# Performance work log

Hardware: AMD Instinct MI355X
Metric: run time of the kernel (lower is better)

Reference implementation:

```python
import jax, jax.numpy as jnp
import numpy as np

LN_EPS = 1e-5
SCALE = 1.0 / 8.0  # 1/sqrt(dim/num_heads) = 1/sqrt(64)


def layernorm(x, g, b):
    m = jnp.mean(x, axis=-1, keepdims=True)
    v = jnp.mean(jnp.square(x - m), axis=-1, keepdims=True)
    return (x - m) * jax.lax.rsqrt(v + LN_EPS) * g + b


def attention_block(q_in, kv_in, wq, bq, wk, bk, wv, bv, g, b):
    # un-split single-matrix attention, faithful to the source (no head reshape)
    Q = q_in @ wq + bq            # [B,S,D]
    K = kv_in @ wk + bk           # [B,T,D]
    V = kv_in @ wv + bv           # [B,T,D]
    scores = jnp.einsum('bsd,btd->bst', Q, K) * SCALE  # [B,S,T]
    A = jax.nn.softmax(scores, axis=-1)
    out = jnp.einsum('bst,btd->bsd', A, V)
    return layernorm(out + q_in, g, b)


def setup_inputs() -> dict:
    key = jax.random.key(0)
    ks = jax.random.split(key, 16)
    B, S, T, D = 4, 2048, 2048, 1024
    w = lambda k: jax.random.normal(k, (D, D), dtype=jnp.float32) * 0.02
    z = jnp.zeros((D,), dtype=jnp.float32)
    o = jnp.ones((D,), dtype=jnp.float32)
    return {
        'x': jax.random.normal(ks[0], (B, S, D), dtype=jnp.float32),
        'y': jax.random.normal(ks[1], (B, T, D), dtype=jnp.float32),
        'wq_m': w(ks[2]), 'bq_m': z, 'wk_m': w(ks[3]), 'bk_m': z,
        'wv_m': w(ks[4]), 'bv_m': z, 'g_m': o, 'b_m': z,
        'wq_c': w(ks[5]), 'bq_c': z, 'wk_c': w(ks[6]), 'bk_c': z,
        'wv_c': w(ks[7]), 'bv_c': z, 'g_c': o, 'b_c': z,
        'f0_w': w(ks[8]), 'f0_b': z, 'f1_w': w(ks[9]), 'f1_b': z,
        'g_d': o, 'b_d': z,
    }


def reference(x, y,
              wq_m, bq_m, wk_m, bk_m, wv_m, bv_m, g_m, b_m,
              wq_c, bq_c, wk_c, bk_c, wv_c, bv_c, g_c, b_c,
              f0_w, f0_b, f1_w, f1_b, g_d, b_d):
    # masked (self) attention + shared decoder LN residual
    res = x
    x = layernorm(attention_block(x, x, wq_m, bq_m, wk_m, bk_m, wv_m, bv_m, g_m, b_m) + res, g_d, b_d)
    # cross attention against memory y
    res = x
    x = layernorm(attention_block(x, y, wq_c, bq_c, wk_c, bk_c, wv_c, bv_c, g_c, b_c) + res, g_d, b_d)
    # FFN: loop condition in source is always true -> GELU (exact) after every layer
    res = x
    x = jax.nn.gelu(x @ f0_w + f0_b, approximate=False)
    x = jax.nn.gelu(x @ f1_w + f1_b, approximate=False)
    return layernorm(x + res, g_d, b_d)
```

## Files before the change

### kernel.cpp

```cpp
#include <hip/hip_runtime.h>

#define DEV __device__ __forceinline__

typedef __attribute__((ext_vector_type(8))) short bf16x8;
typedef __attribute__((ext_vector_type(4))) float f32x4;

DEV float bf2f(unsigned short u) { return __uint_as_float(((unsigned int)u) << 16); }
DEV unsigned short f2bf(float f) {
    unsigned int x = __float_as_uint(f);
    return (unsigned short)((x + 0x7fffu + ((x >> 16) & 1u)) >> 16);
}
DEV float gelu_exact(float x) { return 0.5f * x * (1.0f + erff(x * 0.7071067811865475f)); }

DEV void gload16(const void* g, void* l) {
    __builtin_amdgcn_global_load_lds((const __attribute__((address_space(1))) void*)g,
                                     (__attribute__((address_space(3))) void*)l, 16, 0, 0);
}

template <int OFF>
DEV bf16x8 ds_read128(unsigned addr) {
    bf16x8 r;
    asm volatile("ds_read_b128 %0, %1 offset:%2" : "=v"(r) : "v"(addr), "i"(OFF));
    return r;
}

__global__ __launch_bounds__(256) void transpose_cast_w(const float* __restrict__ in,
                                                        unsigned short* __restrict__ out,
                                                        int R, int C) {
    __shared__ float tile[32][33];
    int c0 = blockIdx.x * 32, r0 = blockIdx.y * 32;
    int tx = threadIdx.x, ty = threadIdx.y;
#pragma unroll
    for (int i = 0; i < 32; i += 8)
        tile[ty + i][tx] = in[(size_t)(r0 + ty + i) * C + (c0 + tx)];
    __syncthreads();
#pragma unroll
    for (int i = 0; i < 32; i += 8)
        out[(size_t)(c0 + ty + i) * R + (r0 + tx)] = f2bf(tile[tx][ty + i]);
}

__global__ __launch_bounds__(256) void cast_f32_bf16(const float* __restrict__ in,
                                                     unsigned short* __restrict__ out, int n4) {
    int i = blockIdx.x * 256 + threadIdx.x;
    if (i >= n4) return;
    float4 v = ((const float4*)in)[i];
    unsigned short o[4] = {f2bf(v.x), f2bf(v.y), f2bf(v.z), f2bf(v.w)};
    *(uint2*)(out + (size_t)i * 4) = *(uint2*)o;
}


template <int H>
DEV void mfma32(const bf16x8 (&a)[4][2], const bf16x8 (&b)[4][2], f32x4 (&acc)[8][4]) {
#pragma unroll
    for (int ks = 0; ks < 2; ++ks)
#pragma unroll
        for (int mi = 0; mi < 4; ++mi)
#pragma unroll
            for (int n = 0; n < 4; ++n)
                acc[4 * H + mi][n] =
                    __builtin_amdgcn_mfma_f32_16x16x32_bf16(a[mi][ks], b[n][ks], acc[4 * H + mi][n], 0, 0, 0);
}

template <int BIAS_MODE, bool GELU_ACT, bool OUT_F32>
__global__ __launch_bounds__(512, 2) void gemm256(const unsigned short* __restrict__ A,
                                                  const unsigned short* __restrict__ BT,
                                                  const float* __restrict__ bias,
                                                  float* __restrict__ Cf,
                                                  unsigned short* __restrict__ Cb,
                                                  int N, int K, int lda, int ldb, float scale,
                                                  long sA, long sB, long sC, long sBias) {
    const int gx = gridDim.x, gy = gridDim.y;
    int f = blockIdx.x + gx * (blockIdx.y + gy * blockIdx.z);
    const int nwg = gx * gy * gridDim.z;
    f = (f & 7) * (nwg >> 3) + (f >> 3);
    const int bz = f / (gx * gy);
    const int rem = f - bz * gx * gy;
    const int by = rem / gx;
    const int bx = rem - by * gx;

    A += (long)bz * sA;
    BT += (long)bz * sB;
    if (BIAS_MODE) bias += (long)bz * sBias;

    const int tid = threadIdx.x;
    const int lane = tid & 63;
    const int wave = tid >> 6;
    const int wm = wave >> 2;
    const int wn = wave & 3;
    const int llo = lane & 15, lhi = lane >> 4;
    const int bm = bx * 256, bn = by * 256;
    const int brow = (wn & 1) * 64;

    __shared__ unsigned short lds[2][4][128 * 64];

    const int xk0 = (0 + lhi) ^ (llo & 7);
    const int xk1 = (4 + lhi) ^ (llo & 7);

    const unsigned ldsA = (unsigned)(size_t)&lds[0][wm][0] + (unsigned)llo * 128u;
    const unsigned ldsB = (unsigned)(size_t)&lds[0][2 + (wn >> 1)][0] + (unsigned)(brow + llo) * 128u;
    unsigned aA[2][2], aB[2][2];
    aA[0][0] = ldsA + xk0 * 16; aA[0][1] = ldsA + xk1 * 16;
    aA[1][0] = aA[0][0] + 65536u; aA[1][1] = aA[0][1] + 65536u;
    aB[0][0] = ldsB + xk0 * 16; aB[0][1] = ldsB + xk1 * 16;
    aB[1][0] = aB[0][0] + 65536u; aB[1][1] = aB[0][1] + 65536u;

    const int d0 = wave * 64 + lane;
    const int sr0 = d0 >> 3, sq0 = (d0 & 7) ^ (sr0 & 7);
    const int d1 = 512 + d0;
    const int sr1 = d1 >> 3, sq1 = (d1 & 7) ^ (sr1 & 7);

    const unsigned short* gA0 = A + (size_t)bm * lda;
    const unsigned short* gA1 = A + (size_t)(bm + 128) * lda;
    const unsigned short* gB0 = BT + (size_t)bn * ldb;
    const unsigned short* gB1 = BT + (size_t)(bn + 128) * ldb;

#define STAGE(grow, ld, kt, l)                                                          \
    {                                                                                   \
        gload16((grow) + (size_t)sr0 * (ld) + (kt) + sq0 * 8, (l) + wave * 512);        \
        gload16((grow) + (size_t)sr1 * (ld) + (kt) + sq1 * 8, (l) + 4096 + wave * 512); \
    }
#define SA(kt, BUF) { STAGE(gA0, lda, kt, lds[BUF][0]); STAGE(gA1, lda, kt, lds[BUF][1]); }
#define SB(kt, BUF) { STAGE(gB0, ldb, kt, lds[BUF][2]); STAGE(gB1, ldb, kt, lds[BUF][3]); }

    f32x4 acc[8][4] = {};
    bf16x8 b[4][2];

#define PH2(H, BUF, LOADB, STG, TAIL)                                        \
    {                                                                        \
        STG;                                                                 \
        bf16x8 afr[4][2];                                                    \
        afr[0][0] = ds_read128<(H)*8192 + 0>(aA[BUF][0]);                    \
        afr[0][1] = ds_read128<(H)*8192 + 0>(aA[BUF][1]);                    \
        afr[1][0] = ds_read128<(H)*8192 + 2048>(aA[BUF][0]);                 \
        afr[1][1] = ds_read128<(H)*8192 + 2048>(aA[BUF][1]);                 \
        afr[2][0] = ds_read128<(H)*8192 + 4096>(aA[BUF][0]);                 \
        afr[2][1] = ds_read128<(H)*8192 + 4096>(aA[BUF][1]);                 \
        afr[3][0] = ds_read128<(H)*8192 + 6144>(aA[BUF][0]);                 \
        afr[3][1] = ds_read128<(H)*8192 + 6144>(aA[BUF][1]);                 \
        if (LOADB) {                                                         \
            b[0][0] = ds_read128<0>(aB[BUF][0]);                             \
            b[0][1] = ds_read128<0>(aB[BUF][1]);                             \
            b[1][0] = ds_read128<2048>(aB[BUF][0]);                          \
            b[1][1] = ds_read128<2048>(aB[BUF][1]);                          \
            b[2][0] = ds_read128<4096>(aB[BUF][0]);                          \
            b[2][1] = ds_read128<4096>(aB[BUF][1]);                          \
            b[3][0] = ds_read128<6144>(aB[BUF][0]);                          \
            b[3][1] = ds_read128<6144>(aB[BUF][1]);                          \
        }                                                                    \
        __builtin_amdgcn_s_barrier();                                        \
        asm volatile("s_waitcnt lgkmcnt(0)" :::);                            \
        __builtin_amdgcn_sched_barrier(0);                                   \
        __builtin_amdgcn_s_setprio(1);                                       \
        mfma32<H>(afr, b, acc);                                              \
        __builtin_amdgcn_s_setprio(0);                                       \
        TAIL;                                                                \
        __builtin_amdgcn_s_barrier();                                        \
    }

#define VM4 asm volatile("s_waitcnt vmcnt(4)" :::)
#define VM0 asm volatile("s_waitcnt vmcnt(0)" :::)
#define NOP ((void)0)

    const int nt = K >> 6;
    const int niter = nt >> 1;

    SA(0, 0);
    SB(0, 0);
    SB(64, 1);
    VM4;
    __builtin_amdgcn_s_barrier();

    int kt = 0;
    for (int i = 0; i < niter - 1; ++i) {
        const int kt1 = kt + 64, kt2 = kt + 128, kt3 = kt + 192;
        PH2(0, 0, true,  SA(kt1, 1), NOP);
        PH2(1, 0, false, SB(kt2, 0), VM4);
        PH2(0, 1, true,  SA(kt2, 0), NOP);
        PH2(1, 1, false, SB(kt3, 1), VM4);
        kt += 128;
    }
    {
        const int kt1 = kt + 64;
        PH2(0, 0, true,  SA(kt1, 1), NOP);
        PH2(1, 0, false, NOP, VM0);
        PH2(0, 1, true,  NOP, NOP);
        PH2(1, 1, false, NOP, NOP);
    }
#undef PH2
#undef SA
#undef SB
#undef STAGE
#undef VM4
#undef VM0
#undef NOP

#pragma unroll
    for (int m = 0; m < 8; ++m) {
#pragma unroll
        for (int n = 0; n < 4; ++n) {
            const int col = bn + wn * 64 + n * 16 + llo;
            float bcol = 0.f;
            if constexpr (BIAS_MODE == 1) bcol = bias[col];
#pragma unroll
            for (int j = 0; j < 4; ++j) {
                const int row = bm + wm * 128 + m * 16 + lhi * 4 + j;
                float v = acc[m][n][j] * scale + bcol;
                if constexpr (BIAS_MODE == 2) v += bias[row];
                if constexpr (GELU_ACT) v = gelu_exact(v);
                const size_t idx = (size_t)bz * (size_t)sC + (size_t)row * N + col;
                if constexpr (OUT_F32) Cf[idx] = v;
                else Cb[idx] = f2bf(v);
            }
        }
    }
}

__global__ __launch_bounds__(256) void softmax_rows(unsigned short* __restrict__ s, int T) {
    __shared__ float red[4];
    unsigned short* p = s + (size_t)blockIdx.x * T;
    const int tid = threadIdx.x;

    uint4 raw = *(const uint4*)(p + tid * 8);
    const unsigned short* u = (const unsigned short*)&raw;
    float v[8];
#pragma unroll
    for (int j = 0; j < 8; ++j) v[j] = bf2f(u[j]);

    float mx = -3.4e38f;
#pragma unroll
    for (int j = 0; j < 8; ++j) mx = fmaxf(mx, v[j]);
#pragma unroll
    for (int o = 32; o; o >>= 1) mx = fmaxf(mx, __shfl_xor(mx, o));
    if ((tid & 63) == 0) red[tid >> 6] = mx;
    __syncthreads();
    mx = fmaxf(fmaxf(red[0], red[1]), fmaxf(red[2], red[3]));
    __syncthreads();

    float sum = 0.f;
#pragma unroll
    for (int j = 0; j < 8; ++j) {
        v[j] = expf(v[j] - mx);
        sum += v[j];
    }
#pragma unroll
    for (int o = 32; o; o >>= 1) sum += __shfl_xor(sum, o);
    if ((tid & 63) == 0) red[tid >> 6] = sum;
    __syncthreads();
    sum = red[0] + red[1] + red[2] + red[3];
    const float inv = 1.0f / sum;

    unsigned short o8[8];
#pragma unroll
    for (int j = 0; j < 8; ++j) o8[j] = f2bf(v[j] * inv);
    *(uint4*)(p + tid * 8) = *(uint4*)o8;
}

DEV float block_sum(float v, float* red, int tid) {
#pragma unroll
    for (int o = 32; o; o >>= 1) v += __shfl_xor(v, o);
    if ((tid & 63) == 0) red[tid >> 6] = v;
    __syncthreads();
    v = red[0] + red[1] + red[2] + red[3];
    __syncthreads();
    return v;
}

__global__ __launch_bounds__(256) void ln_double(const float* __restrict__ av,
                                                 const float* __restrict__ xin,
                                                 const float* __restrict__ g1, const float* __restrict__ b1,
                                                 const float* __restrict__ g2, const float* __restrict__ b2,
                                                 float* __restrict__ xout,
                                                 unsigned short* __restrict__ xbf, int D) {
    __shared__ float red[4];
    const int tid = threadIdx.x;
    const size_t base = (size_t)blockIdx.x * D + tid * 4;
    const float4 a4 = *(const float4*)(av + base);
    const float4 x4 = *(const float4*)(xin + base);
    float x[4] = {x4.x, x4.y, x4.z, x4.w};
    float t[4] = {a4.x + x[0], a4.y + x[1], a4.z + x[2], a4.w + x[3]};
    const float invD = 1.0f / D;

    float m = block_sum(t[0] + t[1] + t[2] + t[3], red, tid) * invD;
    float q = 0.f;
#pragma unroll
    for (int j = 0; j < 4; ++j) q += (t[j] - m) * (t[j] - m);
    q = block_sum(q, red, tid) * invD;
    float rs = rsqrtf(q + 1e-5f);

    float u[4];
#pragma unroll
    for (int j = 0; j < 4; ++j) {
        const int idx = tid * 4 + j;
        u[j] = (t[j] - m) * rs * g1[idx] + b1[idx] + x[j];
    }
    float m2 = block_sum(u[0] + u[1] + u[2] + u[3], red, tid) * invD;
    float q2 = 0.f;
#pragma unroll
    for (int j = 0; j < 4; ++j) q2 += (u[j] - m2) * (u[j] - m2);
    q2 = block_sum(q2, red, tid) * invD;
    float rs2 = rsqrtf(q2 + 1e-5f);

    float4 o4;
    unsigned short ob[4];
#pragma unroll
    for (int j = 0; j < 4; ++j) {
        const int idx = tid * 4 + j;
        float o = (u[j] - m2) * rs2 * g2[idx] + b2[idx];
        ((float*)&o4)[j] = o;
        ob[j] = f2bf(o);
    }
    *(float4*)(xout + base) = o4;
    *(uint2*)(xbf + base) = *(uint2*)ob;
}

__global__ __launch_bounds__(256) void ln_single(const float* __restrict__ a,
                                                 const float* __restrict__ b_,
                                                 const float* __restrict__ g, const float* __restrict__ bb,
                                                 float* __restrict__ out, int D) {
    __shared__ float red[4];
    const int tid = threadIdx.x;
    const size_t base = (size_t)blockIdx.x * D + tid * 4;
    const float4 a4 = *(const float4*)(a + base);
    const float4 x4 = *(const float4*)(b_ + base);
    float t[4] = {a4.x + x4.x, a4.y + x4.y, a4.z + x4.z, a4.w + x4.w};
    const float invD = 1.0f / D;
    float m = block_sum(t[0] + t[1] + t[2] + t[3], red, tid) * invD;
    float q = 0.f;
#pragma unroll
    for (int j = 0; j < 4; ++j) q += (t[j] - m) * (t[j] - m);
    q = block_sum(q, red, tid) * invD;
    float rs = rsqrtf(q + 1e-5f);
    float4 o4;
#pragma unroll
    for (int j = 0; j < 4; ++j) {
        const int idx = tid * 4 + j;
        ((float*)&o4)[j] = (t[j] - m) * rs * g[idx] + bb[idx];
    }
    *(float4*)(out + base) = o4;
}

extern "C" void kernel_launch(void* const* d_in, const int* in_sizes, int n_in,
                              void* d_out, int out_size, void* d_ws, size_t ws_size,
                              hipStream_t stream) {
    (void)in_sizes; (void)n_in; (void)out_size; (void)ws_size;
    constexpr int B = 4, S = 2048, T = 2048, D = 1024;
    constexpr int M = B * S;
    constexpr long MD = (long)M * D;
    constexpr long ST = (long)S * T;
    constexpr long DD = (long)D * D;

    const float* x = (const float*)d_in[0];
    const float* y = (const float*)d_in[1];
    const float* w_in[8] = {(const float*)d_in[2],  (const float*)d_in[4],  (const float*)d_in[6],
                            (const float*)d_in[10], (const float*)d_in[12], (const float*)d_in[14],
                            (const float*)d_in[18], (const float*)d_in[20]};
    const float* bq_m = (const float*)d_in[3];
    const float* bk_m = (const float*)d_in[5];
    const float* bv_m = (const float*)d_in[7];
    const float* g_m = (const float*)d_in[8];
    const float* b_m = (const float*)d_in[9];
    const float* bq_c = (const float*)d_in[11];
    const float* bk_c = (const float*)d_in[13];
    const float* bv_c = (const float*)d_in[15];
    const float* g_c = (const float*)d_in[16];
    const float* b_c = (const float*)d_in[17];
    const float* f0_b = (const float*)d_in[19];
    const float* f1_b = (const float*)d_in[21];
    const float* g_d = (const float*)d_in[22];
    const float* b_d = (const float*)d_in[23];
    float* dout = (float*)d_out;

    char* p = (char*)d_ws;
    auto carve = [&](size_t bytes) { void* r = p; p += (bytes + 255) & ~(size_t)255; return r; };
    float* xcur = (float*)carve(MD * 4);
    unsigned short* wT = (unsigned short*)carve((size_t)8 * DD * 2);
    unsigned short* abf = (unsigned short*)carve(MD * 2);
    unsigned short* ybf = (unsigned short*)carve(MD * 2);
    unsigned short* Qb = (unsigned short*)carve(MD * 2);
    unsigned short* Kb = (unsigned short*)carve(MD * 2);
    unsigned short* Vt = (unsigned short*)carve(MD * 2);
    unsigned short* scores = (unsigned short*)carve((size_t)B * ST * 2);
    float* tmp = (float*)carve(MD * 4);
    float* bqk_m = (float*)carve(2 * D * 4);
    float* bqk_c = (float*)carve(2 * D * 4);

    const dim3 blk256(256), blk512(512);
    const dim3 tb(32, 8);

    for (int w = 0; w < 8; ++w)
        transpose_cast_w<<<dim3(32, 32), tb, 0, stream>>>(w_in[w], wT + (size_t)w * DD, D, D);
    cast_f32_bf16<<<dim3(M * D / 4 / 256), blk256, 0, stream>>>(x, abf, M * D / 4);
    cast_f32_bf16<<<dim3(M * D / 4 / 256), blk256, 0, stream>>>(y, ybf, M * D / 4);
    hipMemcpyAsync(bqk_m, bq_m, D * 4, hipMemcpyDeviceToDevice, stream);
    hipMemcpyAsync(bqk_m + D, bk_m, D * 4, hipMemcpyDeviceToDevice, stream);
    hipMemcpyAsync(bqk_c, bq_c, D * 4, hipMemcpyDeviceToDevice, stream);
    hipMemcpyAsync(bqk_c + D, bk_c, D * 4, hipMemcpyDeviceToDevice, stream);

    unsigned short* wqm = wT + 0 * DD;
    unsigned short* wvm = wT + 2 * DD;
    unsigned short* wqc = wT + 3 * DD;
    unsigned short* wvc = wT + 5 * DD;
    unsigned short* wf0 = wT + 6 * DD;
    unsigned short* wf1 = wT + 7 * DD;

    const dim3 gQK(M / 256, D / 256, 2);
    const dim3 gVt(D / 256, T / 256, B);
    const dim3 gScores(S / 256, T / 256, B);
    const dim3 gPV(S / 256, D / 256, B);
    const dim3 gFFN(M / 256, D / 256, 1);

    gemm256<1, false, false><<<gQK, blk512, 0, stream>>>(abf, wqm, bqk_m, nullptr, Qb, D, D, D, D, 1.f, 0, DD, MD, D);
    gemm256<2, false, false><<<gVt, blk512, 0, stream>>>(wvm, abf, bv_m, nullptr, Vt, T, D, D, D, 1.f, 0, (long)S * D, (long)D * T, 0);
    gemm256<0, false, false><<<gScores, blk512, 0, stream>>>(Qb, Kb, nullptr, nullptr, scores, T, D, D, D, 0.125f, (long)S * D, (long)T * D, ST, 0);
    softmax_rows<<<dim3(B * S), blk256, 0, stream>>>(scores, T);
    gemm256<0, false, true><<<gPV, blk512, 0, stream>>>(scores, Vt, nullptr, tmp, nullptr, D, T, T, T, 1.f, ST, (long)T * D, (long)S * D, 0);
    ln_double<<<dim3(M), blk256, 0, stream>>>(tmp, x, g_m, b_m, g_d, b_d, xcur, abf, D);

    gemm256<1, false, false><<<gQK, blk512, 0, stream>>>(abf, wqc, bqk_c, nullptr, Qb, D, D, D, D, 1.f, MD, DD, MD, D);
    gemm256<2, false, false><<<gVt, blk512, 0, stream>>>(wvc, ybf, bv_c, nullptr, Vt, T, D, D, D, 1.f, 0, (long)S * D, (long)D * T, 0);
    gemm256<0, false, false><<<gScores, blk512, 0, stream>>>(Qb, Kb, nullptr, nullptr, scores, T, D, D, D, 0.125f, (long)S * D, (long)T * D, ST, 0);
    softmax_rows<<<dim3(B * S), blk256, 0, stream>>>(scores, T);
    gemm256<0, false, true><<<gPV, blk512, 0, stream>>>(scores, Vt, nullptr, tmp, nullptr, D, T, T, T, 1.f, ST, (long)T * D, (long)S * D, 0);
    ln_double<<<dim3(M), blk256, 0, stream>>>(tmp, xcur, g_c, b_c, g_d, b_d, xcur, abf, D);

    gemm256<1, true, false><<<gFFN, blk512, 0, stream>>>(abf, wf0, f0_b, nullptr, Qb, D, D, D, D, 1.f, 0, 0, 0, 0);
    gemm256<1, true, true><<<gFFN, blk512, 0, stream>>>(Qb, wf1, f1_b, tmp, nullptr, D, D, D, D, 1.f, 0, 0, 0, 0);
    ln_single<<<dim3(M), blk256, 0, stream>>>(tmp, xcur, g_d, b_d, dout, D);
}
```

Before: 576.3 us.

## Replace 256x256 GEMM tile with 128x128 four-wave kernel

```diff
diff --git a/kernel.cpp b/kernel.cpp
--- a/kernel.cpp
+++ b/kernel.cpp
@@ -50,19 +50,18 @@
 
 
 template <int H>
-DEV void mfma32(const bf16x8 (&a)[4][2], const bf16x8 (&b)[4][2], f32x4 (&acc)[8][4]) {
+DEV void mfma16q(const bf16x8 (&a)[2][2], const bf16x8 (&b)[4][2], f32x4 (&acc)[4][4]) {
 #pragma unroll
     for (int ks = 0; ks < 2; ++ks)
 #pragma unroll
-        for (int mi = 0; mi < 4; ++mi)
-#pragma unroll
-            for (int n = 0; n < 4; ++n)
-                acc[4 * H + mi][n] =
-                    __builtin_amdgcn_mfma_f32_16x16x32_bf16(a[mi][ks], b[n][ks], acc[4 * H + mi][n], 0, 0, 0);
+        for (int n = 0; n < 4; ++n) {
+            acc[2 * H][n]     = __builtin_amdgcn_mfma_f32_16x16x32_bf16(a[0][ks], b[n][ks], acc[2 * H][n], 0, 0, 0);
+            acc[2 * H + 1][n] = __builtin_amdgcn_mfma_f32_16x16x32_bf16(a[1][ks], b[n][ks], acc[2 * H + 1][n], 0, 0, 0);
+        }
 }
 
 template <int BIAS_MODE, bool GELU_ACT, bool OUT_F32>
-__global__ __launch_bounds__(512, 2) void gemm256(const unsigned short* __restrict__ A,
+__global__ __launch_bounds__(256, 2) void gemm128(const unsigned short* __restrict__ A,
                                                   const unsigned short* __restrict__ BT,
                                                   const float* __restrict__ bias,
                                                   float* __restrict__ Cf,
@@ -85,125 +84,112 @@
     const int tid = threadIdx.x;
     const int lane = tid & 63;
     const int wave = tid >> 6;
-    const int wm = wave >> 2;
-    const int wn = wave & 3;
+    const int wr = wave >> 1;
+    const int wc = wave & 1;
     const int llo = lane & 15, lhi = lane >> 4;
-    const int bm = bx * 256, bn = by * 256;
-    const int brow = (wn & 1) * 64;
-
-    __shared__ unsigned short lds[2][4][128 * 64];
+    const int bm = bx * 128, bn = by * 128;
+
+    __shared__ unsigned short lds[2][2][128 * 64];
 
     const int xk0 = (0 + lhi) ^ (llo & 7);
     const int xk1 = (4 + lhi) ^ (llo & 7);
 
-    const unsigned ldsA = (unsigned)(size_t)&lds[0][wm][0] + (unsigned)llo * 128u;
-    const unsigned ldsB = (unsigned)(size_t)&lds[0][2 + (wn >> 1)][0] + (unsigned)(brow + llo) * 128u;
-    unsigned aA[2][2], aB[2][2];
-    aA[0][0] = ldsA + xk0 * 16; aA[0][1] = ldsA + xk1 * 16;
-    aA[1][0] = aA[0][0] + 65536u; aA[1][1] = aA[0][1] + 65536u;
-    aB[0][0] = ldsB + xk0 * 16; aB[0][1] = ldsB + xk1 * 16;
-    aB[1][0] = aB[0][0] + 65536u; aB[1][1] = aB[0][1] + 65536u;
-
-    const int d0 = wave * 64 + lane;
-    const int sr0 = d0 >> 3, sq0 = (d0 & 7) ^ (sr0 & 7);
-    const int d1 = 512 + d0;
-    const int sr1 = d1 >> 3, sq1 = (d1 & 7) ^ (sr1 & 7);
-
-    const unsigned short* gA0 = A + (size_t)bm * lda;
-    const unsigned short* gA1 = A + (size_t)(bm + 128) * lda;
-    const unsigned short* gB0 = BT + (size_t)bn * ldb;
-    const unsigned short* gB1 = BT + (size_t)(bn + 128) * ldb;
-
-#define STAGE(grow, ld, kt, l)                                                          \
+    const unsigned base0 = (unsigned)(size_t)&lds[0][0][0];
+    const unsigned aA0 = base0 + (unsigned)(wr * 64 + llo) * 128u + xk0 * 16;
+    const unsigned aA1 = base0 + (unsigned)(wr * 64 + llo) * 128u + xk1 * 16;
+    const unsigned aB0 = base0 + (unsigned)(wc * 64 + llo) * 128u + xk0 * 16;
+    const unsigned aB1 = base0 + (unsigned)(wc * 64 + llo) * 128u + xk1 * 16;
+
+    int srow[4], sq[4];
+#pragma unroll
+    for (int L = 0; L < 4; ++L) {
+        const int d = L * 256 + tid;
+        srow[L] = d >> 3;
+        sq[L] = (d & 7) ^ (srow[L] & 7);
+    }
+    const unsigned short* gA = A + (size_t)bm * lda;
+    const unsigned short* gB = BT + (size_t)bn * ldb;
+
+#define SA(kt, BUF)                                                                     \
     {                                                                                   \
-        gload16((grow) + (size_t)sr0 * (ld) + (kt) + sq0 * 8, (l) + wave * 512);        \
-        gload16((grow) + (size_t)sr1 * (ld) + (kt) + sq1 * 8, (l) + 4096 + wave * 512); \
-    }
-#define SA(kt, BUF) { STAGE(gA0, lda, kt, lds[BUF][0]); STAGE(gA1, lda, kt, lds[BUF][1]); }
-#define SB(kt, BUF) { STAGE(gB0, ldb, kt, lds[BUF][2]); STAGE(gB1, ldb, kt, lds[BUF][3]); }
-
-    f32x4 acc[8][4] = {};
+        _Pragma("unroll") for (int L = 0; L < 4; ++L)                                   \
+            gload16(gA + (size_t)srow[L] * lda + (kt) + sq[L] * 8,                      \
+                    &lds[BUF][0][(L * 256 + wave * 64) * 8]);                           \
+    }
+#define SB(kt, BUF)                                                                     \
+    {                                                                                   \
+        _Pragma("unroll") for (int L = 0; L < 4; ++L)                                   \
+            gload16(gB + (size_t)srow[L] * ldb + (kt) + sq[L] * 8,                      \
+                    &lds[BUF][1][(L * 256 + wave * 64) * 8]);                           \
+    }
+
+    f32x4 acc[4][4] = {};
     bf16x8 b[4][2];
 
-#define PH2(H, BUF, LOADB, STG, TAIL)                                        \
+#define PH(H, BUF, LOADB, STG, TAIL)                                         \
     {                                                                        \
         STG;                                                                 \
-        bf16x8 afr[4][2];                                                    \
-        afr[0][0] = ds_read128<(H)*8192 + 0>(aA[BUF][0]);                    \
-        afr[0][1] = ds_read128<(H)*8192 + 0>(aA[BUF][1]);                    \
-        afr[1][0] = ds_read128<(H)*8192 + 2048>(aA[BUF][0]);                 \
-        afr[1][1] = ds_read128<(H)*8192 + 2048>(aA[BUF][1]);                 \
-        afr[2][0] = ds_read128<(H)*8192 + 4096>(aA[BUF][0]);                 \
-        afr[2][1] = ds_read128<(H)*8192 + 4096>(aA[BUF][1]);                 \
-        afr[3][0] = ds_read128<(H)*8192 + 6144>(aA[BUF][0]);                 \
-        afr[3][1] = ds_read128<(H)*8192 + 6144>(aA[BUF][1]);                 \
+        bf16x8 afr[2][2];                                                    \
+        afr[0][0] = ds_read128<(BUF)*32768 + (H)*4096 + 0>(aA0);             \
+        afr[0][1] = ds_read128<(BUF)*32768 + (H)*4096 + 0>(aA1);             \
+        afr[1][0] = ds_read128<(BUF)*32768 + (H)*4096 + 2048>(aA0);          \
+        afr[1][1] = ds_read128<(BUF)*32768 + (H)*4096 + 2048>(aA1);          \
         if (LOADB) {                                                         \
-            b[0][0] = ds_read128<0>(aB[BUF][0]);                             \
-            b[0][1] = ds_read128<0>(aB[BUF][1]);                             \
-            b[1][0] = ds_read128<2048>(aB[BUF][0]);                          \
-            b[1][1] = ds_read128<2048>(aB[BUF][1]);                          \
-            b[2][0] = ds_read128<4096>(aB[BUF][0]);                          \
-            b[2][1] = ds_read128<4096>(aB[BUF][1]);                          \
-            b[3][0] = ds_read128<6144>(aB[BUF][0]);                          \
-            b[3][1] = ds_read128<6144>(aB[BUF][1]);                          \
+            b[0][0] = ds_read128<(BUF)*32768 + 16384 + 0>(aB0);              \
+            b[0][1] = ds_read128<(BUF)*32768 + 16384 + 0>(aB1);              \
+            b[1][0] = ds_read128<(BUF)*32768 + 16384 + 2048>(aB0);           \
+            b[1][1] = ds_read128<(BUF)*32768 + 16384 + 2048>(aB1);           \
+            b[2][0] = ds_read128<(BUF)*32768 + 16384 + 4096>(aB0);           \
+            b[2][1] = ds_read128<(BUF)*32768 + 16384 + 4096>(aB1);           \
+            b[3][0] = ds_read128<(BUF)*32768 + 16384 + 6144>(aB0);           \
+            b[3][1] = ds_read128<(BUF)*32768 + 16384 + 6144>(aB1);           \
         }                                                                    \
         __builtin_amdgcn_s_barrier();                                        \
         asm volatile("s_waitcnt lgkmcnt(0)" :::);                            \
         __builtin_amdgcn_sched_barrier(0);                                   \
         __builtin_amdgcn_s_setprio(1);                                       \
-        mfma32<H>(afr, b, acc);                                              \
+        mfma16q<H>(afr, b, acc);                                             \
         __builtin_amdgcn_s_setprio(0);                                       \
         TAIL;                                                                \
         __builtin_amdgcn_s_barrier();                                        \
     }
 
-#define VM4 asm volatile("s_waitcnt vmcnt(4)" :::)
 #define VM0 asm volatile("s_waitcnt vmcnt(0)" :::)
 #define NOP ((void)0)
 
     const int nt = K >> 6;
-    const int niter = nt >> 1;
 
     SA(0, 0);
     SB(0, 0);
-    SB(64, 1);
-    VM4;
+    VM0;
     __builtin_amdgcn_s_barrier();
 
     int kt = 0;
-    for (int i = 0; i < niter - 1; ++i) {
-        const int kt1 = kt + 64, kt2 = kt + 128, kt3 = kt + 192;
-        PH2(0, 0, true,  SA(kt1, 1), NOP);
-        PH2(1, 0, false, SB(kt2, 0), VM4);
-        PH2(0, 1, true,  SA(kt2, 0), NOP);
-        PH2(1, 1, false, SB(kt3, 1), VM4);
+    for (int t = 0; t < nt; t += 2) {
+        const bool st0 = (t + 1 < nt);
+        const bool st1 = (t + 2 < nt);
+        PH(0, 0, true,  if (st0) { SA(kt + 64, 1); SB(kt + 64, 1); }, NOP);
+        PH(1, 0, false, NOP, VM0);
+        PH(0, 1, true,  if (st1) { SA(kt + 128, 0); SB(kt + 128, 0); }, NOP);
+        PH(1, 1, false, NOP, VM0);
         kt += 128;
     }
-    {
-        const int kt1 = kt + 64;
-        PH2(0, 0, true,  SA(kt1, 1), NOP);
-        PH2(1, 0, false, NOP, VM0);
-        PH2(0, 1, true,  NOP, NOP);
-        PH2(1, 1, false, NOP, NOP);
-    }
-#undef PH2
+#undef PH
 #undef SA
 #undef SB
-#undef STAGE
-#undef VM4
 #undef VM0
 #undef NOP
 
 #pragma unroll
-    for (int m = 0; m < 8; ++m) {
+    for (int m = 0; m < 4; ++m) {
 #pragma unroll
         for (int n = 0; n < 4; ++n) {
-            const int col = bn + wn * 64 + n * 16 + llo;
+            const int col = bn + wc * 64 + n * 16 + llo;
             float bcol = 0.f;
             if constexpr (BIAS_MODE == 1) bcol = bias[col];
 #pragma unroll
             for (int j = 0; j < 4; ++j) {
-                const int row = bm + wm * 128 + m * 16 + lhi * 4 + j;
+                const int row = bm + wr * 64 + m * 16 + lhi * 4 + j;
                 float v = acc[m][n][j] * scale + bcol;
                 if constexpr (BIAS_MODE == 2) v += bias[row];
                 if constexpr (GELU_ACT) v = gelu_exact(v);
@@ -384,7 +370,7 @@
     float* bqk_m = (float*)carve(2 * D * 4);
     float* bqk_c = (float*)carve(2 * D * 4);
 
-    const dim3 blk256(256), blk512(512);
+    const dim3 blk256(256);
     const dim3 tb(32, 8);
 
     for (int w = 0; w < 8; ++w)
@@ -403,27 +389,27 @@
     unsigned short* wf0 = wT + 6 * DD;
     unsigned short* wf1 = wT + 7 * DD;
 
-    const dim3 gQK(M / 256, D / 256, 2);
-    const dim3 gVt(D / 256, T / 256, B);
-    const dim3 gScores(S / 256, T / 256, B);
-    const dim3 gPV(S / 256, D / 256, B);
-    const dim3 gFFN(M / 256, D / 256, 1);
-
-    gemm256<1, false, false><<<gQK, blk512, 0, stream>>>(abf, wqm, bqk_m, nullptr, Qb, D, D, D, D, 1.f, 0, DD, MD, D);
-    gemm256<2, false, false><<<gVt, blk512, 0, stream>>>(wvm, abf, bv_m, nullptr, Vt, T, D, D, D, 1.f, 0, (long)S * D, (long)D * T, 0);
-    gemm256<0, false, false><<<gScores, blk512, 0, stream>>>(Qb, Kb, nullptr, nullptr, scores, T, D, D, D, 0.125f, (long)S * D, (long)T * D, ST, 0);
+    const dim3 gQK(M / 128, D / 128, 2);
+    const dim3 gVt(D / 128, T / 128, B);
+    const dim3 gScores(S / 128, T / 128, B);
+    const dim3 gPV(S / 128, D / 128, B);
+    const dim3 gFFN(M / 128, D / 128, 1);
+
+    gemm128<1, false, false><<<gQK, blk256, 0, stream>>>(abf, wqm, bqk_m, nullptr, Qb, D, D, D, D, 1.f, 0, DD, MD, D);
+    gemm128<2, false, false><<<gVt, blk256, 0, stream>>>(wvm, abf, bv_m, nullptr, Vt, T, D, D, D, 1.f, 0, (long)S * D, (long)D * T, 0);
+    gemm128<0, false, false><<<gScores, blk256, 0, stream>>>(Qb, Kb, nullptr, nullptr, scores, T, D, D, D, 0.125f, (long)S * D, (long)T * D, ST, 0);
     softmax_rows<<<dim3(B * S), blk256, 0, stream>>>(scores, T);
-    gemm256<0, false, true><<<gPV, blk512, 0, stream>>>(scores, Vt, nullptr, tmp, nullptr, D, T, T, T, 1.f, ST, (long)T * D, (long)S * D, 0);
+    gemm128<0, false, true><<<gPV, blk256, 0, stream>>>(scores, Vt, nullptr, tmp, nullptr, D, T, T, T, 1.f, ST, (long)T * D, (long)S * D, 0);
     ln_double<<<dim3(M), blk256, 0, stream>>>(tmp, x, g_m, b_m, g_d, b_d, xcur, abf, D);
 
-    gemm256<1, false, false><<<gQK, blk512, 0, stream>>>(abf, wqc, bqk_c, nullptr, Qb, D, D, D, D, 1.f, MD, DD, MD, D);
-    gemm256<2, false, false><<<gVt, blk512, 0, stream>>>(wvc, ybf, bv_c, nullptr, Vt, T, D, D, D, 1.f, 0, (long)S * D, (long)D * T, 0);
-    gemm256<0, false, false><<<gScores, blk512, 0, stream>>>(Qb, Kb, nullptr, nullptr, scores, T, D, D, D, 0.125f, (long)S * D, (long)T * D, ST, 0);
+    gemm128<1, false, false><<<gQK, blk256, 0, stream>>>(abf, wqc, bqk_c, nullptr, Qb, D, D, D, D, 1.f, MD, DD, MD, D);
+    gemm128<2, false, false><<<gVt, blk256, 0, stream>>>(wvc, ybf, bv_c, nullptr, Vt, T, D, D, D, 1.f, 0, (long)S * D, (long)D * T, 0);
+    gemm128<0, false, false><<<gScores, blk256, 0, stream>>>(Qb, Kb, nullptr, nullptr, scores, T, D, D, D, 0.125f, (long)S * D, (long)T * D, ST, 0);
     softmax_rows<<<dim3(B * S), blk256, 0, stream>>>(scores, T);
-    gemm256<0, false, true><<<gPV, blk512, 0, stream>>>(scores, Vt, nullptr, tmp, nullptr, D, T, T, T, 1.f, ST, (long)T * D, (long)S * D, 0);
+    gemm128<0, false, true><<<gPV, blk256, 0, stream>>>(scores, Vt, nullptr, tmp, nullptr, D, T, T, T, 1.f, ST, (long)T * D, (long)S * D, 0);
     ln_double<<<dim3(M), blk256, 0, stream>>>(tmp, xcur, g_c, b_c, g_d, b_d, xcur, abf, D);
 
-    gemm256<1, true, false><<<gFFN, blk512, 0, stream>>>(abf, wf0, f0_b, nullptr, Qb, D, D, D, D, 1.f, 0, 0, 0, 0);
-    gemm256<1, true, true><<<gFFN, blk512, 0, stream>>>(Qb, wf1, f1_b, tmp, nullptr, D, D, D, D, 1.f, 0, 0, 0, 0);
+    gemm128<1, true, false><<<gFFN, blk256, 0, stream>>>(abf, wf0, f0_b, nullptr, Qb, D, D, D, D, 1.f, 0, 0, 0, 0);
+    gemm128<1, true, true><<<gFFN, blk256, 0, stream>>>(Qb, wf1, f1_b, tmp, nullptr, D, D, D, D, 1.f, 0, 0, 0, 0);
     ln_single<<<dim3(M), blk256, 0, stream>>>(tmp, xcur, g_d, b_d, dout, D);
 }
```

New measurement: 496.6 us. 1.16x faster.
